# Kernel tuning notes

Measured on AMD Instinct MI355X. Metric: run time of the kernel, lower is better.

Reference implementation:

```python
import jax, jax.numpy as jnp
import numpy as np

D_MODEL = 4096
NUM_EXPERTS = 64
TOP_K = 8


def setup_inputs() -> dict:
    key = jax.random.key(0)
    kx, kw = jax.random.split(key)
    x = jax.random.normal(kx, (4, 4096, D_MODEL), dtype=jnp.float32)
    # nn.Linear weight [num_experts, d_model]; y = x @ W.T
    W = jax.random.normal(kw, (NUM_EXPERTS, D_MODEL), dtype=jnp.float32) * (1.0 / np.sqrt(D_MODEL))
    return {"x": x, "W": W}


def reference(x, W):
    # logits: [b, s, e]
    logits = jnp.einsum('bsd,ed->bse', x, W)
    router_probs = jax.nn.softmax(logits, axis=-1)
    top_k_weights, top_k_indices = jax.lax.top_k(router_probs, TOP_K)
    top_k_weights = top_k_weights / (jnp.sum(top_k_weights, axis=-1, keepdims=True) + 1e-9)
    return top_k_weights, top_k_indices, router_probs
```

## Files before the change

kernel.cpp:

```cpp
#include <hip/hip_runtime.h>
#include <math.h>

#define D_MODEL 4096
#define NEXP    64
#define TOPK    8
#define NTOK    16384
#define BLK_TOK 64
#define KSPLIT  4
#define KQ      (D_MODEL / KSPLIT)
#define R_GRID  ((NTOK / BLK_TOK) * KSPLIT)

#define W2_USHORTS (NEXP * D_MODEL * 2)

typedef __attribute__((ext_vector_type(8))) short bf16x8;
typedef __attribute__((ext_vector_type(4))) float f32x4;

__device__ inline unsigned b16rne(float f) {
    unsigned u = __float_as_uint(f);
    return (u + 0x7FFFu + ((u >> 16) & 1u)) >> 16;
}

__global__ void transpose_w_kernel(const float* __restrict__ W, unsigned short* __restrict__ W2,
                                   float* __restrict__ out_p, int* __restrict__ cnt) {
    int o = blockIdx.x * 256 + threadIdx.x;
    int i  = o & 7;
    int e  = (o >> 3) & 63;
    int kb = o >> 9;
    float w = W[(size_t)e * D_MODEL + kb * 8 + i];
    unsigned hb = b16rne(w);
    float hf = __uint_as_float(hb << 16);
    unsigned lb = b16rne(w - hf);
    size_t base = ((size_t)(kb * 64 + e) * 2) * 8 + i;
    W2[base]     = (unsigned short)hb;
    W2[base + 8] = (unsigned short)lb;
    *(float4*)&out_p[(size_t)o * 4] = make_float4(0.f, 0.f, 0.f, 0.f);
    if (o == 0) *cnt = 0;
}

__global__ __launch_bounds__(256)
void router_kernel(const float* __restrict__ x, const unsigned short* __restrict__ W2,
                   float* __restrict__ Pacc) {
    __shared__ float lg[BLK_TOK * 65];

    const int tid  = threadIdx.x;
    const int lane = tid & 63;
    const int wv   = __builtin_amdgcn_readfirstlane(tid >> 6);

    const int nb   = (blockIdx.x & 7) * (R_GRID / 8) + (blockIdx.x >> 3);
    const int s    = nb & 3;
    const int tok0 = (nb >> 2) * BLK_TOK;
    const int kbase = s * KQ;

    const int l15 = lane & 15;
    const int kg  = lane >> 4;

    f32x4 acc[4];
#pragma unroll
    for (int nt = 0; nt < 4; ++nt) acc[nt] = (f32x4)0.f;

    const float* xrow = x + (size_t)(tok0 + wv * 16 + l15) * D_MODEL + kbase + kg * 8;
    const unsigned short* wbase = W2 + ((size_t)(((kbase >> 3) + kg) * 64 + l15) * 2) * 8;

    for (int ks = 0; ks < KQ / 32; ++ks) {
        const float4 xa = *(const float4*)(xrow + ks * 32);
        const float4 xb = *(const float4*)(xrow + ks * 32 + 4);

        union { unsigned u[4]; bf16x8 v; } Ahi, Alo;
#pragma unroll
        for (int p = 0; p < 4; ++p) {
            const float f0 = (p == 0) ? xa.x : (p == 1) ? xa.z : (p == 2) ? xb.x : xb.z;
            const float f1 = (p == 0) ? xa.y : (p == 1) ? xa.w : (p == 2) ? xb.y : xb.w;
            const unsigned h0 = b16rne(f0), h1 = b16rne(f1);
            Ahi.u[p] = h0 | (h1 << 16);
            const float l0 = f0 - __uint_as_float(h0 << 16);
            const float l1 = f1 - __uint_as_float(h1 << 16);
            Alo.u[p] = b16rne(l0) | (b16rne(l1) << 16);
        }

        const unsigned short* wk = wbase + (size_t)ks * 4096;
#pragma unroll
        for (int nt = 0; nt < 4; ++nt) {
            const unsigned short* wp = wk + nt * 256;
            const bf16x8 bhi = *(const bf16x8*)(wp);
            const bf16x8 blo = *(const bf16x8*)(wp + 8);
            acc[nt] = __builtin_amdgcn_mfma_f32_16x16x32_bf16(Ahi.v, bhi, acc[nt], 0, 0, 0);
            acc[nt] = __builtin_amdgcn_mfma_f32_16x16x32_bf16(Ahi.v, blo, acc[nt], 0, 0, 0);
            acc[nt] = __builtin_amdgcn_mfma_f32_16x16x32_bf16(Alo.v, bhi, acc[nt], 0, 0, 0);
        }
    }

#pragma unroll
    for (int nt = 0; nt < 4; ++nt)
#pragma unroll
        for (int r = 0; r < 4; ++r)
            lg[(wv * 16 + kg * 4 + r) * 65 + nt * 16 + l15] = acc[nt][r];
    __syncthreads();

    for (int i = tid; i < BLK_TOK * 16; i += 256) {
        const int t  = i >> 4;
        const int e4 = (i & 15) << 2;
        const float* src = &lg[t * 65 + e4];
        float* dst = &Pacc[(size_t)(tok0 + t) * NEXP + e4];
#pragma unroll
        for (int c = 0; c < 4; ++c) atomicAdd(dst + c, src[c]);
    }
}

__global__ __launch_bounds__(256)
void finalize_kernel(float* out_p, float* __restrict__ out_w, float* __restrict__ out_i,
                     int* __restrict__ cnt, int* __restrict__ list) {
    __shared__ float lg[BLK_TOK * 65];
    const int tid  = threadIdx.x;
    const int tok0 = blockIdx.x * BLK_TOK;

    for (int i = tid; i < BLK_TOK * 16; i += 256) {
        const int t  = i >> 4;
        const int e4 = (i & 15) << 2;
        const float4 a = *(const float4*)&out_p[(size_t)(tok0 + t) * NEXP + e4];
        float* dst = &lg[t * 65 + e4];
        dst[0] = a.x; dst[1] = a.y; dst[2] = a.z; dst[3] = a.w;
    }
    __syncthreads();

    if (tid < 64) {
        const int tok = tok0 + tid;
        float p[64];
        float m = -INFINITY;
#pragma unroll
        for (int e = 0; e < 64; ++e) {
            p[e] = lg[tid * 65 + e];
            m = fmaxf(m, p[e]);
        }
        float z = 0.f;
#pragma unroll
        for (int e = 0; e < 64; ++e) {
            p[e] = __expf(p[e] - m);
            z += p[e];
        }
        const float rz = 1.f / z;
#pragma unroll
        for (int e = 0; e < 64; ++e) {
            p[e] *= rz;
            lg[tid * 65 + e] = p[e];
        }

        float tv[9]; int ti[9];
#pragma unroll
        for (int k = 0; k < 9; ++k) { tv[k] = -1.f; ti[k] = 0; }
        for (int e = 0; e < 64; ++e) {
            float v = p[e]; int idx = e;
#pragma unroll
            for (int k = 0; k < 9; ++k) {
                const bool gt = v > tv[k];
                const float nv = gt ? v : tv[k];
                const int   ni = gt ? idx : ti[k];
                const float ov = gt ? tv[k] : v;
                const int   oi = gt ? ti[k] : idx;
                tv[k] = nv; ti[k] = ni; v = ov; idx = oi;
            }
        }
        int flag = 0;
#pragma unroll
        for (int k = 0; k < 8; ++k)
            if (tv[k] - tv[k + 1] <= tv[k] * 4e-4f + 1e-9f) flag = 1;
        if (flag) {
            int sidx = atomicAdd(cnt, 1);
            list[sidx] = tok;
        }

        float s8 = 0.f;
#pragma unroll
        for (int k = 0; k < 8; ++k) s8 += tv[k];
        const float denom = s8 + 1e-9f;
#pragma unroll
        for (int k = 0; k < 8; ++k) {
            out_w[tok * TOPK + k] = tv[k] / denom;
            out_i[tok * TOPK + k] = (float)ti[k];
        }
    }
    __syncthreads();

    for (int i = tid; i < BLK_TOK * 16; i += 256) {
        const int t  = i >> 4;
        const int e4 = (i & 15) << 2;
        const float* src = &lg[t * 65 + e4];
        *(float4*)&out_p[(size_t)(tok0 + t) * NEXP + e4] =
            make_float4(src[0], src[1], src[2], src[3]);
    }
}

__global__ __launch_bounds__(256)
void repair_kernel(const float* __restrict__ x, const float* __restrict__ W,
                   const int* __restrict__ cnt, const int* __restrict__ list,
                   float* __restrict__ out_w, float* __restrict__ out_i) {
    __shared__ float  xs[D_MODEL];
    __shared__ double ls[4][NEXP];
    const int tid = threadIdx.x;
    const int e   = tid & 63;
    const int w4  = tid >> 6;
    const int n   = cnt[0];

    for (int i = blockIdx.x; i < n; i += gridDim.x) {
        const int tok = list[i];
        __syncthreads();
        const float4* xsrc = (const float4*)(x + (size_t)tok * D_MODEL);
        for (int v = tid; v < D_MODEL / 4; v += 256)
            ((float4*)xs)[v] = xsrc[v];
        __syncthreads();

        const float* wrow = W + (size_t)e * D_MODEL + w4 * (D_MODEL / 4);
        const float* xrow = xs + w4 * (D_MODEL / 4);
        double s0 = 0., s1 = 0., s2 = 0., s3 = 0.;
        for (int d = 0; d < D_MODEL / 4; d += 4) {
            const float4 wv = *(const float4*)(wrow + d);
            const float4 xv = *(const float4*)(xrow + d);
            s0 += (double)xv.x * (double)wv.x;
            s1 += (double)xv.y * (double)wv.y;
            s2 += (double)xv.z * (double)wv.z;
            s3 += (double)xv.w * (double)wv.w;
        }
        ls[w4][e] = (s0 + s1) + (s2 + s3);
        __syncthreads();

        if (tid == 0) {
            double lsum[64];
            for (int k = 0; k < 64; ++k)
                lsum[k] = (ls[0][k] + ls[1][k]) + (ls[2][k] + ls[3][k]);
            double m = -1e300;
            for (int k = 0; k < 64; ++k) m = lsum[k] > m ? lsum[k] : m;
            double p[64], Z = 0.;
            for (int k = 0; k < 64; ++k) { p[k] = exp(lsum[k] - m); Z += p[k]; }
            for (int k = 0; k < 64; ++k) p[k] /= Z;

            double tv[8]; int ti[8];
            for (int k = 0; k < 8; ++k) { tv[k] = -1.; ti[k] = 0; }
            for (int k = 0; k < 64; ++k) {
                double v = p[k]; int idx = k;
                for (int u = 0; u < 8; ++u) {
                    const bool gt = v > tv[u];
                    const double nv = gt ? v : tv[u];
                    const int    ni = gt ? idx : ti[u];
                    const double ov = gt ? tv[u] : v;
                    const int    oi = gt ? ti[u] : idx;
                    tv[u] = nv; ti[u] = ni; v = ov; idx = oi;
                }
            }
            double s8 = 0.;
            for (int k = 0; k < 8; ++k) s8 += tv[k];
            const double denom = s8 + 1e-9;
            for (int k = 0; k < 8; ++k) {
                out_w[tok * TOPK + k] = (float)(tv[k] / denom);
                out_i[tok * TOPK + k] = (float)ti[k];
            }
        }
    }
}

extern "C" void kernel_launch(void* const* d_in, const int* in_sizes, int n_in,
                              void* d_out, int out_size, void* d_ws, size_t ws_size,
                              hipStream_t stream) {
    const float* x = (const float*)d_in[0];
    const float* W = (const float*)d_in[1];

    unsigned short* W2 = (unsigned short*)d_ws;
    int* cnt  = (int*)(W2 + W2_USHORTS);
    int* list = cnt + 1;

    float* out   = (float*)d_out;
    float* out_w = out;
    float* out_i = out + NTOK * TOPK;
    float* out_p = out + 2 * NTOK * TOPK;

    transpose_w_kernel<<<262144 / 256, 256, 0, stream>>>(W, W2, out_p, cnt);
    router_kernel<<<R_GRID, 256, 0, stream>>>(x, W2, out_p);
    finalize_kernel<<<NTOK / BLK_TOK, 256, 0, stream>>>(out_p, out_w, out_i, cnt, list);
    repair_kernel<<<256, 256, 0, stream>>>(x, W, cnt, list, out_w, out_i);
}
```

Measured before the change: 538.7 us.

## Fuse router GEMM, softmax/top-k finalize and fp64 repair into one 1024-thread kernel

Replaces the split-K router with global atomics, the separate finalize kernel and the repair kernel with a single kernel. Each 1024-thread block handles 64 tokens, and its 16 waves split K four ways. Partial logits are reduced in shared memory, after which the block runs softmax and top-k, and recomputes flagged near-tie tokens in fp64 within the same block. This removes the atomics, the zeroing of the probability buffer, the global counter and list, and three launches. In exchange the grid shrinks to 256 blocks, the block does a serialized per-token repair, and the four-phase LDS reduction adds barriers.

```diff
diff --git a/kernel.cpp b/kernel.cpp
--- a/kernel.cpp
+++ b/kernel.cpp
@@ -6,9 +6,8 @@
 #define TOPK    8
 #define NTOK    16384
 #define BLK_TOK 64
-#define KSPLIT  4
-#define KQ      (D_MODEL / KSPLIT)
-#define R_GRID  ((NTOK / BLK_TOK) * KSPLIT)
+#define NTHR    1024
+#define KC      1024
 
 #define W2_USHORTS (NEXP * D_MODEL * 2)
 
@@ -20,8 +19,7 @@
     return (u + 0x7FFFu + ((u >> 16) & 1u)) >> 16;
 }
 
-__global__ void transpose_w_kernel(const float* __restrict__ W, unsigned short* __restrict__ W2,
-                                   float* __restrict__ out_p, int* __restrict__ cnt) {
+__global__ void prep_kernel(const float* __restrict__ W, unsigned short* __restrict__ W2) {
     int o = blockIdx.x * 256 + threadIdx.x;
     int i  = o & 7;
     int e  = (o >> 3) & 63;
@@ -33,23 +31,26 @@
     size_t base = ((size_t)(kb * 64 + e) * 2) * 8 + i;
     W2[base]     = (unsigned short)hb;
     W2[base + 8] = (unsigned short)lb;
-    *(float4*)&out_p[(size_t)o * 4] = make_float4(0.f, 0.f, 0.f, 0.f);
-    if (o == 0) *cnt = 0;
-}
-
-__global__ __launch_bounds__(256)
+}
+
+__global__ __launch_bounds__(NTHR)
 void router_kernel(const float* __restrict__ x, const unsigned short* __restrict__ W2,
-                   float* __restrict__ Pacc) {
-    __shared__ float lg[BLK_TOK * 65];
+                   const float* __restrict__ W,
+                   float* __restrict__ out_w, float* __restrict__ out_i,
+                   float* __restrict__ out_p) {
+    __shared__ float  lg[BLK_TOK * 65];
+    __shared__ float  xs[D_MODEL];
+    __shared__ double ls[16][NEXP];
+    __shared__ int    flg[BLK_TOK];
+    __shared__ double sm2;
 
     const int tid  = threadIdx.x;
     const int lane = tid & 63;
     const int wv   = __builtin_amdgcn_readfirstlane(tid >> 6);
-
-    const int nb   = (blockIdx.x & 7) * (R_GRID / 8) + (blockIdx.x >> 3);
-    const int s    = nb & 3;
-    const int tok0 = (nb >> 2) * BLK_TOK;
-    const int kbase = s * KQ;
+    const int tw   = wv & 3;
+    const int kw   = wv >> 2;
+    const int tok0 = blockIdx.x * BLK_TOK;
+    const int kbase = kw * KC;
 
     const int l15 = lane & 15;
     const int kg  = lane >> 4;
@@ -58,10 +59,11 @@
 #pragma unroll
     for (int nt = 0; nt < 4; ++nt) acc[nt] = (f32x4)0.f;
 
-    const float* xrow = x + (size_t)(tok0 + wv * 16 + l15) * D_MODEL + kbase + kg * 8;
+    const float* xrow = x + (size_t)(tok0 + tw * 16 + l15) * D_MODEL + kbase + kg * 8;
     const unsigned short* wbase = W2 + ((size_t)(((kbase >> 3) + kg) * 64 + l15) * 2) * 8;
 
-    for (int ks = 0; ks < KQ / 32; ++ks) {
+#pragma unroll 2
+    for (int ks = 0; ks < KC / 32; ++ks) {
         const float4 xa = *(const float4*)(xrow + ks * 32);
         const float4 xb = *(const float4*)(xrow + ks * 32 + 4);
 
@@ -89,66 +91,41 @@
         }
     }
 
-#pragma unroll
-    for (int nt = 0; nt < 4; ++nt)
-#pragma unroll
-        for (int r = 0; r < 4; ++r)
-            lg[(wv * 16 + kg * 4 + r) * 65 + nt * 16 + l15] = acc[nt][r];
-    __syncthreads();
-
-    for (int i = tid; i < BLK_TOK * 16; i += 256) {
-        const int t  = i >> 4;
-        const int e4 = (i & 15) << 2;
-        const float* src = &lg[t * 65 + e4];
-        float* dst = &Pacc[(size_t)(tok0 + t) * NEXP + e4];
-#pragma unroll
-        for (int c = 0; c < 4; ++c) atomicAdd(dst + c, src[c]);
-    }
-}
-
-__global__ __launch_bounds__(256)
-void finalize_kernel(float* out_p, float* __restrict__ out_w, float* __restrict__ out_i,
-                     int* __restrict__ cnt, int* __restrict__ list) {
-    __shared__ float lg[BLK_TOK * 65];
-    const int tid  = threadIdx.x;
-    const int tok0 = blockIdx.x * BLK_TOK;
-
-    for (int i = tid; i < BLK_TOK * 16; i += 256) {
-        const int t  = i >> 4;
-        const int e4 = (i & 15) << 2;
-        const float4 a = *(const float4*)&out_p[(size_t)(tok0 + t) * NEXP + e4];
-        float* dst = &lg[t * 65 + e4];
-        dst[0] = a.x; dst[1] = a.y; dst[2] = a.z; dst[3] = a.w;
-    }
-    __syncthreads();
+    for (int p = 0; p < 4; ++p) {
+        if (kw == p) {
+#pragma unroll
+            for (int nt = 0; nt < 4; ++nt)
+#pragma unroll
+                for (int r = 0; r < 4; ++r) {
+                    float* c = &lg[(tw * 16 + kg * 4 + r) * 65 + nt * 16 + l15];
+                    if (p == 0) *c = acc[nt][r];
+                    else       *c += acc[nt][r];
+                }
+        }
+        __syncthreads();
+    }
 
     if (tid < 64) {
         const int tok = tok0 + tid;
-        float p[64];
         float m = -INFINITY;
 #pragma unroll
+        for (int e = 0; e < 64; ++e) m = fmaxf(m, lg[tid * 65 + e]);
+        float z = 0.f;
+#pragma unroll
         for (int e = 0; e < 64; ++e) {
-            p[e] = lg[tid * 65 + e];
-            m = fmaxf(m, p[e]);
-        }
-        float z = 0.f;
-#pragma unroll
-        for (int e = 0; e < 64; ++e) {
-            p[e] = __expf(p[e] - m);
-            z += p[e];
+            const float pe = __expf(lg[tid * 65 + e] - m);
+            z += pe;
+            lg[tid * 65 + e] = pe;
         }
         const float rz = 1.f / z;
 #pragma unroll
-        for (int e = 0; e < 64; ++e) {
-            p[e] *= rz;
-            lg[tid * 65 + e] = p[e];
-        }
+        for (int e = 0; e < 64; ++e) lg[tid * 65 + e] *= rz;
 
         float tv[9]; int ti[9];
 #pragma unroll
         for (int k = 0; k < 9; ++k) { tv[k] = -1.f; ti[k] = 0; }
         for (int e = 0; e < 64; ++e) {
-            float v = p[e]; int idx = e;
+            float v = lg[tid * 65 + e]; int idx = e;
 #pragma unroll
             for (int k = 0; k < 9; ++k) {
                 const bool gt = v > tv[k];
@@ -163,10 +140,7 @@
 #pragma unroll
         for (int k = 0; k < 8; ++k)
             if (tv[k] - tv[k + 1] <= tv[k] * 4e-4f + 1e-9f) flag = 1;
-        if (flag) {
-            int sidx = atomicAdd(cnt, 1);
-            list[sidx] = tok;
-        }
+        flg[tid] = flag;
 
         float s8 = 0.f;
 #pragma unroll
@@ -180,62 +154,62 @@
     }
     __syncthreads();
 
-    for (int i = tid; i < BLK_TOK * 16; i += 256) {
-        const int t  = i >> 4;
-        const int e4 = (i & 15) << 2;
+    {
+        const int t  = tid >> 4;
+        const int e4 = (tid & 15) << 2;
         const float* src = &lg[t * 65 + e4];
         *(float4*)&out_p[(size_t)(tok0 + t) * NEXP + e4] =
             make_float4(src[0], src[1], src[2], src[3]);
     }
-}
-
-__global__ __launch_bounds__(256)
-void repair_kernel(const float* __restrict__ x, const float* __restrict__ W,
-                   const int* __restrict__ cnt, const int* __restrict__ list,
-                   float* __restrict__ out_w, float* __restrict__ out_i) {
-    __shared__ float  xs[D_MODEL];
-    __shared__ double ls[4][NEXP];
-    const int tid = threadIdx.x;
-    const int e   = tid & 63;
-    const int w4  = tid >> 6;
-    const int n   = cnt[0];
-
-    for (int i = blockIdx.x; i < n; i += gridDim.x) {
-        const int tok = list[i];
-        __syncthreads();
-        const float4* xsrc = (const float4*)(x + (size_t)tok * D_MODEL);
-        for (int v = tid; v < D_MODEL / 4; v += 256)
+
+    const int e = tid & 63;
+    const int q = tid >> 6;
+    for (int t = 0; t < BLK_TOK; ++t) {
+        if (!flg[t]) continue;
+        __syncthreads();
+        const float4* xsrc = (const float4*)(x + (size_t)(tok0 + t) * D_MODEL);
+        for (int v = tid; v < D_MODEL / 4; v += NTHR)
             ((float4*)xs)[v] = xsrc[v];
         __syncthreads();
 
-        const float* wrow = W + (size_t)e * D_MODEL + w4 * (D_MODEL / 4);
-        const float* xrow = xs + w4 * (D_MODEL / 4);
-        double s0 = 0., s1 = 0., s2 = 0., s3 = 0.;
-        for (int d = 0; d < D_MODEL / 4; d += 4) {
-            const float4 wv = *(const float4*)(wrow + d);
-            const float4 xv = *(const float4*)(xrow + d);
-            s0 += (double)xv.x * (double)wv.x;
-            s1 += (double)xv.y * (double)wv.y;
-            s2 += (double)xv.z * (double)wv.z;
-            s3 += (double)xv.w * (double)wv.w;
-        }
-        ls[w4][e] = (s0 + s1) + (s2 + s3);
-        __syncthreads();
-
+        {
+            const float* wrow = W + (size_t)e * D_MODEL + q * 256;
+            const float* xr2 = xs + q * 256;
+            double s0 = 0., s1 = 0., s2 = 0., s3 = 0.;
+            for (int d = 0; d < 256; d += 4) {
+                const float4 wv2 = *(const float4*)(wrow + d);
+                const float4 xv2 = *(const float4*)(xr2 + d);
+                s0 += (double)xv2.x * (double)wv2.x;
+                s1 += (double)xv2.y * (double)wv2.y;
+                s2 += (double)xv2.z * (double)wv2.z;
+                s3 += (double)xv2.w * (double)wv2.w;
+            }
+            ls[q][e] = (s0 + s1) + (s2 + s3);
+        }
+        __syncthreads();
+
+        if (tid < 64) {
+            double v = 0.;
+#pragma unroll
+            for (int qq = 0; qq < 16; ++qq) v += ls[qq][tid];
+            ls[0][tid] = v;
+        }
+        __syncthreads();
         if (tid == 0) {
-            double lsum[64];
-            for (int k = 0; k < 64; ++k)
-                lsum[k] = (ls[0][k] + ls[1][k]) + (ls[2][k] + ls[3][k]);
             double m = -1e300;
-            for (int k = 0; k < 64; ++k) m = lsum[k] > m ? lsum[k] : m;
-            double p[64], Z = 0.;
-            for (int k = 0; k < 64; ++k) { p[k] = exp(lsum[k] - m); Z += p[k]; }
-            for (int k = 0; k < 64; ++k) p[k] /= Z;
-
+            for (int k = 0; k < 64; ++k) m = ls[0][k] > m ? ls[0][k] : m;
+            sm2 = m;
+        }
+        __syncthreads();
+        if (tid < 64) ls[1][tid] = exp(ls[0][tid] - sm2);
+        __syncthreads();
+        if (tid == 0) {
+            double Z = 0.;
+            for (int k = 0; k < 64; ++k) Z += ls[1][k];
             double tv[8]; int ti[8];
             for (int k = 0; k < 8; ++k) { tv[k] = -1.; ti[k] = 0; }
             for (int k = 0; k < 64; ++k) {
-                double v = p[k]; int idx = k;
+                double v = ls[1][k] / Z; int idx = k;
                 for (int u = 0; u < 8; ++u) {
                     const bool gt = v > tv[u];
                     const double nv = gt ? v : tv[u];
@@ -248,6 +222,7 @@
             double s8 = 0.;
             for (int k = 0; k < 8; ++k) s8 += tv[k];
             const double denom = s8 + 1e-9;
+            const int tok = tok0 + t;
             for (int k = 0; k < 8; ++k) {
                 out_w[tok * TOPK + k] = (float)(tv[k] / denom);
                 out_i[tok * TOPK + k] = (float)ti[k];
@@ -263,16 +238,12 @@
     const float* W = (const float*)d_in[1];
 
     unsigned short* W2 = (unsigned short*)d_ws;
-    int* cnt  = (int*)(W2 + W2_USHORTS);
-    int* list = cnt + 1;
 
     float* out   = (float*)d_out;
     float* out_w = out;
     float* out_i = out + NTOK * TOPK;
     float* out_p = out + 2 * NTOK * TOPK;
 
-    transpose_w_kernel<<<262144 / 256, 256, 0, stream>>>(W, W2, out_p, cnt);
-    router_kernel<<<R_GRID, 256, 0, stream>>>(x, W2, out_p);
-    finalize_kernel<<<NTOK / BLK_TOK, 256, 0, stream>>>(out_p, out_w, out_i, cnt, list);
-    repair_kernel<<<256, 256, 0, stream>>>(x, W, cnt, list, out_w, out_i);
-}
+    prep_kernel<<<262144 / 256, 256, 0, stream>>>(W, W2);
+    router_kernel<<<NTOK / BLK_TOK, NTHR, 0, stream>>>(x, W2, W, out_w, out_i, out_p);
+}
```

Result: slower. 689.8 us (+28.1%).
